# Kernel tuning notes

Measured on AMD Instinct MI355X. Metric: run time of the kernel, lower is better.

## Reference

```python
import jax, jax.numpy as jnp
import numpy as np

SIN, TEMB, EMB, S = 128, 512, 1024, 64
BATCH, T = 4, 4096


def setup_inputs() -> dict:
    key = jax.random.key(0)
    ks = jax.random.split(key, 16)

    def w(k, *shape):
        return jax.random.normal(k, shape, jnp.float32) / np.float32(np.sqrt(shape[0]))

    return {
        "time_embed": jax.random.normal(ks[0], (SIN,), jnp.float32),
        "x": jax.random.normal(ks[1], (BATCH, T, EMB), jnp.float32),
        "W1": w(ks[2], SIN, TEMB), "b1": jnp.zeros((TEMB,), jnp.float32),
        "W2": w(ks[3], TEMB, TEMB), "b2": jnp.zeros((TEMB,), jnp.float32),
        "WA": w(ks[4], TEMB, S), "bA": jnp.zeros((S,), jnp.float32),
        "WB": w(ks[5], TEMB, S, EMB), "bB": jnp.zeros((S, EMB), jnp.float32),
        "WC": w(ks[6], TEMB, EMB, S), "bC": jnp.zeros((EMB, S), jnp.float32),
        "WD": w(ks[7], TEMB, EMB), "bD": jnp.zeros((EMB,), jnp.float32),
        "Wdl": w(ks[8], TEMB, S), "bdl": jnp.zeros((S,), jnp.float32),
        "MA": w(ks[9], SIN, S), "mA": jnp.zeros((S,), jnp.float32),
        "MB": w(ks[10], SIN, S, EMB), "mB": jnp.zeros((S, EMB), jnp.float32),
        "MC": w(ks[11], SIN, EMB, S), "mC": jnp.zeros((EMB, S), jnp.float32),
        "MD": w(ks[12], SIN, EMB), "mD": jnp.zeros((EMB,), jnp.float32),
        "Mdl": w(ks[13], SIN, S), "mdl": jnp.zeros((S,), jnp.float32),
    }


def _ssm_forward(time_embed, x, W1, b1, W2, b2, WA, bA, WB, bB, WC, bC, WD, bD,
                 Wdl, bdl, MA, mA, MB, mB, MC, mC, MD, mD, Mdl, mdl):
    # time-dependent parameter generation
    t = jax.nn.silu(time_embed @ W1 + b1)
    t = t @ W2 + b2  # [TEMB]

    A_base = -jax.nn.softplus(t @ WA + bA)                       # [S]
    B_base = jnp.einsum('t,tse->se', t, WB) + bB                 # [S,E]
    C_base = jnp.einsum('t,tes->es', t, WC) + bC                 # [E,S]
    D_base = t @ WD + bD                                         # [E]
    delta_base = jax.nn.softplus(t @ Wdl + bdl) + 1e-4           # [S]

    A = A_base * jax.nn.sigmoid(time_embed @ MA + mA)
    Bm = B_base * jax.nn.sigmoid(jnp.einsum('t,tse->se', time_embed, MB) + mB)
    C = C_base * jax.nn.sigmoid(jnp.einsum('t,tes->es', time_embed, MC) + mC)
    D = D_base * jax.nn.sigmoid(time_embed @ MD + mD)
    delta = delta_base * jax.nn.sigmoid(time_embed @ Mdl + mdl)  # [S]

    A_bar = jnp.exp(delta * A)          # [S]
    B_bar = delta[:, None] * Bm         # [S,E]

    xt = jnp.swapaxes(x, 0, 1)          # [T,B,E]

    def step(h, x_t):                   # h: [B,S], x_t: [B,E]
        h_new = A_bar * h + x_t @ B_bar.T
        y = h_new @ C.T                 # [B,E]
        return h_new, y

    h0 = jnp.zeros((x.shape[0], A_bar.shape[0]), x.dtype)
    _, ys = jax.lax.scan(step, h0, xt)  # ys: [T,B,E]
    return jnp.swapaxes(ys, 0, 1) + D * x


def reference(time_embed, x, W1, b1, W2, b2, WA, bA, WB, bB, WC, bC, WD, bD,
              Wdl, bdl, MA, mA, MB, mB, MC, mC, MD, mD, Mdl, mdl):
    return _ssm_forward(time_embed, x, W1, b1, W2, b2, WA, bA, WB, bB, WC, bC,
                        WD, bD, Wdl, bdl, MA, mA, MB, mB, MC, mC, MD, mD, Mdl, mdl)
```

## Files before the change

### kernel.cpp

```cpp
#include <hip/hip_runtime.h>
#include <math.h>

#define SIN_ 128
#define TEMB_ 512
#define EMB_ 1024
#define S_ 64
#define B_ 4
#define T_ 4096
#define NROW (B_*T_)
#define L_ 32
#define NC_ (T_/L_)

#define GK 32
#define NSL 16
#define NCH 16
#define NGCH 4

#define WS_T1     0
#define WS_T2     512
#define WS_DELTA  1024
#define WS_ABAR   1088
#define WS_EL     1152
#define WS_FAC    1216
#define WS_D      3264
#define WS_BMTH   4288
#define WS_CTH    37056
#define WS_PD     69824
#define WS_PDG    86208
#define WS_PA     90304
#define WS_PDL    90432
#define WS_PBF    90560
#define WS_HLOCH  90560
#define WS_CHEND  1401280
#define WS_CARRY  1434048

__device__ __forceinline__ float sigmoidf_(float x){ return 1.f/(1.f+expf(-x)); }
__device__ __forceinline__ float softplusf_(float x){ return x>20.f ? x : log1pf(expf(x)); }
__device__ __forceinline__ float4 sig4_(float4 g){
  float4 r; r.x=sigmoidf_(g.x); r.y=sigmoidf_(g.y); r.z=sigmoidf_(g.z); r.w=sigmoidf_(g.w); return r;
}
__device__ __forceinline__ unsigned short f2bf(float x){
  unsigned int u = __float_as_uint(x);
  unsigned int r = (u + 0x7FFFu + ((u>>16)&1u)) >> 16;
  return (unsigned short)r;
}
__device__ __forceinline__ ushort4 pack4(float4 v){
  return make_ushort4(f2bf(v.x),f2bf(v.y),f2bf(v.z),f2bf(v.w));
}
__device__ __forceinline__ float bf2f(unsigned short h){
  return __uint_as_float(((unsigned int)h)<<16);
}

__global__ void k_t1(const float* __restrict__ te, const float* __restrict__ W1,
                     const float* __restrict__ b1, float* __restrict__ ws){
  __shared__ float ste[SIN_];
  int tid = threadIdx.x;
  ste[tid] = te[tid]; ste[tid+64] = te[tid+64];
  __syncthreads();
  int j = blockIdx.x*64 + tid;
  float a = b1[j];
  #pragma unroll 16
  for (int i=0;i<SIN_;i++) a += ste[i]*W1[i*TEMB_ + j];
  ws[WS_T1 + j] = a * sigmoidf_(a);
}

__global__ __launch_bounds__(512) void k_t2(const float* __restrict__ W2,
                                            const float* __restrict__ b2,
                                            float* __restrict__ ws){
  __shared__ float st1[TEMB_];
  __shared__ float red[8][64];
  int tid = threadIdx.x;
  st1[tid] = ws[WS_T1 + tid];
  __syncthreads();
  int jl = tid & 63, kc = tid >> 6;
  int j = blockIdx.x*64 + jl;
  float p = 0.f;
  #pragma unroll 8
  for (int i=0;i<64;i++){
    int k = kc*64 + i;
    p += st1[k]*W2[k*TEMB_ + j];
  }
  red[kc][jl] = p;
  __syncthreads();
  if (tid < 64){
    float a = b2[blockIdx.x*64 + tid];
    #pragma unroll
    for (int c=0;c<8;c++) a += red[c][tid];
    ws[WS_T2 + blockIdx.x*64 + tid] = a;
  }
}

__global__ __launch_bounds__(256,2) void k_partial(
    const float* __restrict__ te,
    const float* __restrict__ WB, const float* __restrict__ MB,
    const float* __restrict__ WC, const float* __restrict__ MC,
    const float* __restrict__ WD, const float* __restrict__ MD,
    const float* __restrict__ WA, const float* __restrict__ MA,
    const float* __restrict__ Wdl, const float* __restrict__ Mdl,
    float* __restrict__ ws){
  __shared__ float st2[TEMB_];
  __shared__ float ste[SIN_];
  int tid = threadIdx.x;
  st2[tid] = ws[WS_T2 + tid];
  st2[tid+256] = ws[WS_T2 + tid + 256];
  if (tid < SIN_) ste[tid] = te[tid];
  __syncthreads();
  unsigned short* pbf = (unsigned short*)(ws + WS_PBF);
  int bb = blockIdx.x;
  if (bb < 512){
    int r = bb>>8, rem = bb&255, j = rem>>4, c = rem&15;
    const float4* W4 = (const float4*)(r ? WC : WB);
    const float4* base = W4 + (size_t)(c*GK)*16384 + j*1024 + tid;
    const float* coef = st2 + c*GK;
    float4 a0={0,0,0,0}, a1={0,0,0,0}, a2={0,0,0,0}, a3={0,0,0,0};
    #pragma unroll 4
    for (int k=0;k<GK;k++){
      const float4* p = base + (size_t)k*16384;
      float4 w0=p[0], w1=p[256], w2=p[512], w3=p[768];
      float cv = coef[k];
      a0.x=fmaf(cv,w0.x,a0.x); a0.y=fmaf(cv,w0.y,a0.y); a0.z=fmaf(cv,w0.z,a0.z); a0.w=fmaf(cv,w0.w,a0.w);
      a1.x=fmaf(cv,w1.x,a1.x); a1.y=fmaf(cv,w1.y,a1.y); a1.z=fmaf(cv,w1.z,a1.z); a1.w=fmaf(cv,w1.w,a1.w);
      a2.x=fmaf(cv,w2.x,a2.x); a2.y=fmaf(cv,w2.y,a2.y); a2.z=fmaf(cv,w2.z,a2.z); a2.w=fmaf(cv,w2.w,a2.w);
      a3.x=fmaf(cv,w3.x,a3.x); a3.y=fmaf(cv,w3.y,a3.y); a3.z=fmaf(cv,w3.z,a3.z); a3.w=fmaf(cv,w3.w,a3.w);
    }
    ushort4* dst = (ushort4*)pbf + (size_t)((r*NSL+j)*NCH + c)*1024;
    dst[tid]     = pack4(a0);
    dst[tid+256] = pack4(a1);
    dst[tid+512] = pack4(a2);
    dst[tid+768] = pack4(a3);
  } else if (bb < 640){
    int g = bb-512, r = g>>6, rem = g&63, j = rem>>2, cg = rem&3;
    const float4* M4 = (const float4*)(r ? MC : MB);
    const float4* base = M4 + (size_t)(cg*GK)*16384 + j*1024 + tid;
    const float* coef = ste + cg*GK;
    float4 a0={0,0,0,0}, a1={0,0,0,0}, a2={0,0,0,0}, a3={0,0,0,0};
    #pragma unroll 4
    for (int k=0;k<GK;k++){
      const float4* p = base + (size_t)k*16384;
      float4 w0=p[0], w1=p[256], w2=p[512], w3=p[768];
      float cv = coef[k];
      a0.x=fmaf(cv,w0.x,a0.x); a0.y=fmaf(cv,w0.y,a0.y); a0.z=fmaf(cv,w0.z,a0.z); a0.w=fmaf(cv,w0.w,a0.w);
      a1.x=fmaf(cv,w1.x,a1.x); a1.y=fmaf(cv,w1.y,a1.y); a1.z=fmaf(cv,w1.z,a1.z); a1.w=fmaf(cv,w1.w,a1.w);
      a2.x=fmaf(cv,w2.x,a2.x); a2.y=fmaf(cv,w2.y,a2.y); a2.z=fmaf(cv,w2.z,a2.z); a2.w=fmaf(cv,w2.w,a2.w);
      a3.x=fmaf(cv,w3.x,a3.x); a3.y=fmaf(cv,w3.y,a3.y); a3.z=fmaf(cv,w3.z,a3.z); a3.w=fmaf(cv,w3.w,a3.w);
    }
    ushort4* dst = (ushort4*)pbf + (size_t)524288 + (size_t)((r*NSL+j)*NGCH + cg)*1024;
    dst[tid]     = pack4(a0);
    dst[tid+256] = pack4(a1);
    dst[tid+512] = pack4(a2);
    dst[tid+768] = pack4(a3);
  } else if (bb < 656){
    int c = bb-640;
    const float4* base = (const float4*)WD + (size_t)(c*GK)*256 + tid;
    const float* coef = st2 + c*GK;
    float4 a={0,0,0,0};
    #pragma unroll 4
    for (int k=0;k<GK;k++){
      float4 w = base[(size_t)k*256];
      float cv = coef[k];
      a.x=fmaf(cv,w.x,a.x); a.y=fmaf(cv,w.y,a.y); a.z=fmaf(cv,w.z,a.z); a.w=fmaf(cv,w.w,a.w);
    }
    ((float4*)(ws + WS_PD))[c*256 + tid] = a;
  } else if (bb < 660){
    int cg = bb-656;
    const float4* base = (const float4*)MD + (size_t)(cg*GK)*256 + tid;
    const float* coef = ste + cg*GK;
    float4 a={0,0,0,0};
    #pragma unroll 4
    for (int k=0;k<GK;k++){
      float4 w = base[(size_t)k*256];
      float cv = coef[k];
      a.x=fmaf(cv,w.x,a.x); a.y=fmaf(cv,w.y,a.y); a.z=fmaf(cv,w.z,a.z); a.w=fmaf(cv,w.w,a.w);
    }
    ((float4*)(ws + WS_PDG))[cg*256 + tid] = a;
  } else {
    const float* Wm = (bb==660) ? WA : Wdl;
    const float* Mm = (bb==660) ? MA : Mdl;
    int outbase = (bb==660) ? WS_PA : WS_PDL;
    __shared__ float red[16][68];
    int q = tid&15, kr = tid>>4;
    float4 acc={0,0,0,0};
    const float4* W4 = (const float4*)Wm;
    #pragma unroll 4
    for (int it=0; it<32; ++it){
      int k = it*16 + kr;
      float4 w = W4[k*16 + q];
      float cv = st2[k];
      acc.x=fmaf(cv,w.x,acc.x); acc.y=fmaf(cv,w.y,acc.y); acc.z=fmaf(cv,w.z,acc.z); acc.w=fmaf(cv,w.w,acc.w);
    }
    red[kr][4*q+0]=acc.x; red[kr][4*q+1]=acc.y; red[kr][4*q+2]=acc.z; red[kr][4*q+3]=acc.w;
    __syncthreads();
    if (tid < 64){
      float s = 0.f;
      #pragma unroll
      for (int g=0;g<16;g++) s += red[g][tid];
      ws[outbase + tid] = s;
    }
    __syncthreads();
    float4 gac={0,0,0,0};
    const float4* M4 = (const float4*)Mm;
    #pragma unroll 4
    for (int it=0; it<8; ++it){
      int k = it*16 + kr;
      float4 w = M4[k*16 + q];
      float cv = ste[k];
      gac.x=fmaf(cv,w.x,gac.x); gac.y=fmaf(cv,w.y,gac.y); gac.z=fmaf(cv,w.z,gac.z); gac.w=fmaf(cv,w.w,gac.w);
    }
    red[kr][4*q+0]=gac.x; red[kr][4*q+1]=gac.y; red[kr][4*q+2]=gac.z; red[kr][4*q+3]=gac.w;
    __syncthreads();
    if (tid < 64){
      float s = 0.f;
      #pragma unroll
      for (int g=0;g<16;g++) s += red[g][tid];
      ws[outbase + 64 + tid] = s;
    }
  }
}

__global__ __launch_bounds__(256) void k_finalize(
    const float* __restrict__ bB, const float* __restrict__ mB,
    const float* __restrict__ bC, const float* __restrict__ mC,
    const float* __restrict__ bD, const float* __restrict__ mD,
    const float* __restrict__ bA_, const float* __restrict__ mA_,
    const float* __restrict__ bdl, const float* __restrict__ mdl,
    float* __restrict__ ws){
  int tid = threadIdx.x, bb = blockIdx.x;
  const ushort4* pbf4 = (const ushort4*)(ws + WS_PBF);
  unsigned short* bmth = (unsigned short*)(ws + WS_BMTH);
  unsigned short* cth  = (unsigned short*)(ws + WS_CTH);
  if (bb < 128){
    int r = bb>>6;
    int q = (bb&63)*256 + tid;
    int j = q>>10, p = q&1023;
    float4 a = {0,0,0,0};
    size_t wbase = ((size_t)(r*NSL+j)*NCH)*1024 + p;
    #pragma unroll
    for (int c=0;c<NCH;c++){
      ushort4 v = pbf4[wbase + (size_t)c*1024];
      a.x += bf2f(v.x); a.y += bf2f(v.y); a.z += bf2f(v.z); a.w += bf2f(v.w);
    }
    float4 g = {0,0,0,0};
    size_t gbase = (size_t)524288 + ((size_t)(r*NSL+j)*NGCH)*1024 + p;
    #pragma unroll
    for (int cg=0;cg<NGCH;cg++){
      ushort4 v = pbf4[gbase + (size_t)cg*1024];
      g.x += bf2f(v.x); g.y += bf2f(v.y); g.z += bf2f(v.z); g.w += bf2f(v.w);
    }
    if (r == 0){
      float4 b4 = ((const float4*)bB)[q];
      float4 m4 = ((const float4*)mB)[q];
      float4 sg = sig4_(make_float4(g.x+m4.x, g.y+m4.y, g.z+m4.z, g.w+m4.w));
      float4 v = make_float4((a.x+b4.x)*sg.x,(a.y+b4.y)*sg.y,(a.z+b4.z)*sg.z,(a.w+b4.w)*sg.w);
      int o = q*4; int s = o>>10; int e = o&1023;
      bmth[(e+0)*64 + s] = f2bf(v.x);
      bmth[(e+1)*64 + s] = f2bf(v.y);
      bmth[(e+2)*64 + s] = f2bf(v.z);
      bmth[(e+3)*64 + s] = f2bf(v.w);
    } else {
      float4 b4 = ((const float4*)bC)[q];
      float4 m4 = ((const float4*)mC)[q];
      float4 sg = sig4_(make_float4(g.x+m4.x, g.y+m4.y, g.z+m4.z, g.w+m4.w));
      float4 v = make_float4((a.x+b4.x)*sg.x,(a.y+b4.y)*sg.y,(a.z+b4.z)*sg.z,(a.w+b4.w)*sg.w);
      int o = q*4; int e = o>>6; int s = o&63;
      cth[(s+0)*1024 + e] = f2bf(v.x);
      cth[(s+1)*1024 + e] = f2bf(v.y);
      cth[(s+2)*1024 + e] = f2bf(v.z);
      cth[(s+3)*1024 + e] = f2bf(v.w);
    }
  } else if (bb == 128){
    float4 a = {0,0,0,0};
    #pragma unroll
    for (int c=0;c<NCH;c++){
      float4 v = ((const float4*)(ws + WS_PD))[c*256 + tid];
      a.x+=v.x; a.y+=v.y; a.z+=v.z; a.w+=v.w;
    }
    float4 g = {0,0,0,0};
    #pragma unroll
    for (int cg=0;cg<NGCH;cg++){
      float4 v = ((const float4*)(ws + WS_PDG))[cg*256 + tid];
      g.x+=v.x; g.y+=v.y; g.z+=v.z; g.w+=v.w;
    }
    float4 b4 = ((const float4*)bD)[tid];
    float4 m4 = ((const float4*)mD)[tid];
    float4 sg = sig4_(make_float4(g.x+m4.x, g.y+m4.y, g.z+m4.z, g.w+m4.w));
    float4 v = make_float4((a.x+b4.x)*sg.x,(a.y+b4.y)*sg.y,(a.z+b4.z)*sg.z,(a.w+b4.w)*sg.w);
    ((float4*)(ws + WS_D))[tid] = v;
  } else {
    __shared__ float sda[64];
    if (tid < 64){
      int s = tid;
      float A = -softplusf_(ws[WS_PA+s] + bA_[s]) * sigmoidf_(ws[WS_PA+64+s] + mA_[s]);
      float delta = (softplusf_(ws[WS_PDL+s] + bdl[s]) + 1e-4f) * sigmoidf_(ws[WS_PDL+64+s] + mdl[s]);
      float da = delta * A;
      sda[s] = da;
      ws[WS_DELTA+s] = delta;
      ws[WS_ABAR+s]  = expf(da);
      ws[WS_EL+s]    = expf((float)L_*da);
    }
    __syncthreads();
    for (int idx=tid; idx<L_*S_; idx+=256){
      int tl = idx>>6, s = idx&63;
      ws[WS_FAC+idx] = expf((float)(tl+1)*sda[s]);
    }
  }
}

__global__ __launch_bounds__(256) void k_scan(const float* __restrict__ x, float* __restrict__ ws){
  __shared__ float Xs[32][68];
  __shared__ float BsT[64][68];
  __shared__ float Us[32][65];
  __shared__ float sdl[S_], sab[S_];
  int tid = threadIdx.x;
  int bb = blockIdx.x;
  int row0 = (bb>>7)*T_ + (bb&127)*L_;
  if (tid<64){ sdl[tid]=ws[WS_DELTA+tid]; sab[tid]=ws[WS_ABAR+tid]; }
  float acc[2][4];
  #pragma unroll
  for (int i=0;i<2;i++)
    #pragma unroll
    for (int j=0;j<4;j++) acc[i][j]=0.f;
  int ty = tid>>4, tx = tid&15;
  const float4* x4 = (const float4*)x;
  const ushort4* bm4 = (const ushort4*)(ws + WS_BMTH);
  for (int kk=0; kk<EMB_; kk+=64){
    #pragma unroll
    for (int t=0;t<2;t++){
      int fl = t*256+tid; int rr = fl>>4, cq = fl&15;
      float4 xv = x4[(size_t)(row0+rr)*256 + (kk>>2) + cq];
      *(float4*)&Xs[rr][cq*4] = xv;
    }
    #pragma unroll
    for (int t=0;t<4;t++){
      int fl = t*256+tid; int rr = fl>>4, cq = fl&15;
      ushort4 hv = bm4[(size_t)(kk+rr)*16 + cq];
      *(float4*)&BsT[rr][cq*4] = make_float4(bf2f(hv.x),bf2f(hv.y),bf2f(hv.z),bf2f(hv.w));
    }
    __syncthreads();
    #pragma unroll 8
    for (int k=0;k<64;k++){
      float4 b4 = *(const float4*)&BsT[k][4*tx];
      float x0 = Xs[2*ty+0][k], x1 = Xs[2*ty+1][k];
      acc[0][0]+=x0*b4.x; acc[0][1]+=x0*b4.y; acc[0][2]+=x0*b4.z; acc[0][3]+=x0*b4.w;
      acc[1][0]+=x1*b4.x; acc[1][1]+=x1*b4.y; acc[1][2]+=x1*b4.z; acc[1][3]+=x1*b4.w;
    }
    __syncthreads();
  }
  #pragma unroll
  for (int i=0;i<2;i++)
    #pragma unroll
    for (int j=0;j<4;j++)
      Us[2*ty+i][4*tx+j] = acc[i][j]*sdl[4*tx+j];
  __syncthreads();
  if (tid<64){
    unsigned short* hh = (unsigned short*)(ws + WS_HLOCH);
    int s = tid; float h = 0.f, ab = sab[s];
    #pragma unroll 8
    for (int t=0;t<L_;t++){
      h = fmaf(ab, h, Us[t][s]);
      hh[(size_t)(row0+t)*S_ + s] = f2bf(h);
    }
    ws[WS_CHEND + bb*S_ + s] = h;
  }
}

__global__ __launch_bounds__(256) void k_carry(float* __restrict__ ws){
  __shared__ float ch[B_*NC_*S_];
  int tid = threadIdx.x;
  const float4* src = (const float4*)(ws + WS_CHEND);
  float4* chv = (float4*)ch;
  for (int i=tid;i<8192;i+=256) chv[i] = src[i];
  __syncthreads();
  int b = tid>>6, s = tid&63;
  float el = ws[WS_EL + s];
  float carry = 0.f;
  #pragma unroll 8
  for (int c=0;c<NC_;c++){
    int idx = (b*NC_ + c)*S_ + s;
    float v = ch[idx];
    ch[idx] = carry;
    carry = fmaf(el, carry, v);
  }
  __syncthreads();
  float4* dst = (float4*)(ws + WS_CARRY);
  for (int i=tid;i<8192;i+=256) dst[i] = chv[i];
}

__global__ __launch_bounds__(256) void k_out(const float* __restrict__ x,
                                             const float* __restrict__ ws,
                                             float* __restrict__ out){
  __shared__ float Cts[64][68];
  __shared__ float Hs[64][68];
  int tid = threadIdx.x;
  int bb = blockIdx.x;
  int rt = bb & 255, et = bb >> 8;
  int row0 = rt*64, e0 = et*64;
  int b = row0 >> 12;
  int cbase = b*NC_ + ((row0 & (T_-1)) >> 5);
  const ushort4* hl4h = (const ushort4*)(ws + WS_HLOCH);
  const ushort4* cth4 = (const ushort4*)(ws + WS_CTH);
  const float4* fc4 = (const float4*)(ws + WS_FAC);
  const float4* cr4 = (const float4*)(ws + WS_CARRY);
  #pragma unroll
  for (int t=0;t<4;t++){
    int fl = t*256+tid; int rr = fl>>4, q = fl&15;
    ushort4 h4 = hl4h[(size_t)(row0+rr)*16 + q];
    float4 f = fc4[(rr & (L_-1))*16 + q];
    float4 c = cr4[(cbase + (rr>>5))*16 + q];
    float4 hv = make_float4(bf2f(h4.x)+f.x*c.x, bf2f(h4.y)+f.y*c.y,
                            bf2f(h4.z)+f.z*c.z, bf2f(h4.w)+f.w*c.w);
    *(float4*)&Hs[rr][q*4] = hv;
    ushort4 ct4 = cth4[(size_t)rr*256 + (e0>>2) + q];
    *(float4*)&Cts[rr][q*4] = make_float4(bf2f(ct4.x),bf2f(ct4.y),bf2f(ct4.z),bf2f(ct4.w));
  }
  __syncthreads();
  int ty = tid>>4, tx = tid&15;
  float acc[4][4];
  #pragma unroll
  for (int i=0;i<4;i++)
    #pragma unroll
    for (int j=0;j<4;j++) acc[i][j]=0.f;
  #pragma unroll 8
  for (int s=0;s<64;s++){
    float4 c4 = *(const float4*)&Cts[s][4*tx];
    float h0 = Hs[4*ty+0][s], h1 = Hs[4*ty+1][s], h2 = Hs[4*ty+2][s], h3 = Hs[4*ty+3][s];
    acc[0][0]+=h0*c4.x; acc[0][1]+=h0*c4.y; acc[0][2]+=h0*c4.z; acc[0][3]+=h0*c4.w;
    acc[1][0]+=h1*c4.x; acc[1][1]+=h1*c4.y; acc[1][2]+=h1*c4.z; acc[1][3]+=h1*c4.w;
    acc[2][0]+=h2*c4.x; acc[2][1]+=h2*c4.y; acc[2][2]+=h2*c4.z; acc[2][3]+=h2*c4.w;
    acc[3][0]+=h3*c4.x; acc[3][1]+=h3*c4.y; acc[3][2]+=h3*c4.z; acc[3][3]+=h3*c4.w;
  }
  float4 d4 = ((const float4*)(ws + WS_D))[(e0>>2) + tx];
  #pragma unroll
  for (int i=0;i<4;i++){
    int row = row0 + 4*ty + i;
    float4 x4v = reinterpret_cast<const float4*>(x + (size_t)row*EMB_ + e0)[tx];
    float4 o;
    o.x = acc[i][0] + d4.x*x4v.x;
    o.y = acc[i][1] + d4.y*x4v.y;
    o.z = acc[i][2] + d4.z*x4v.z;
    o.w = acc[i][3] + d4.w*x4v.w;
    reinterpret_cast<float4*>(out + (size_t)row*EMB_ + e0)[tx] = o;
  }
}

extern "C" void kernel_launch(void* const* d_in, const int* in_sizes, int n_in,
                              void* d_out, int out_size, void* d_ws, size_t ws_size,
                              hipStream_t stream){
  const float* te  = (const float*)d_in[0];
  const float* x   = (const float*)d_in[1];
  const float* W1  = (const float*)d_in[2];
  const float* b1  = (const float*)d_in[3];
  const float* W2  = (const float*)d_in[4];
  const float* b2  = (const float*)d_in[5];
  const float* WA  = (const float*)d_in[6];
  const float* bA  = (const float*)d_in[7];
  const float* WB  = (const float*)d_in[8];
  const float* bB  = (const float*)d_in[9];
  const float* WC  = (const float*)d_in[10];
  const float* bC  = (const float*)d_in[11];
  const float* WD  = (const float*)d_in[12];
  const float* bD  = (const float*)d_in[13];
  const float* Wdl = (const float*)d_in[14];
  const float* bdl = (const float*)d_in[15];
  const float* MA  = (const float*)d_in[16];
  const float* mA  = (const float*)d_in[17];
  const float* MB  = (const float*)d_in[18];
  const float* mB  = (const float*)d_in[19];
  const float* MC  = (const float*)d_in[20];
  const float* mC  = (const float*)d_in[21];
  const float* MD  = (const float*)d_in[22];
  const float* mD  = (const float*)d_in[23];
  const float* Mdl = (const float*)d_in[24];
  const float* mdl = (const float*)d_in[25];
  float* ws  = (float*)d_ws;
  float* out = (float*)d_out;

  k_t1<<<8,64,0,stream>>>(te, W1, b1, ws);
  k_t2<<<8,512,0,stream>>>(W2, b2, ws);
  k_partial<<<662,256,0,stream>>>(te, WB,MB, WC,MC, WD,MD, WA,MA, Wdl,Mdl, ws);
  k_finalize<<<130,256,0,stream>>>(bB,mB, bC,mC, bD,mD, bA,mA, bdl,mdl, ws);
  k_scan<<<512,256,0,stream>>>(x, ws);
  k_carry<<<1,256,0,stream>>>(ws);
  k_out<<<4096,256,0,stream>>>(x, ws, out);
}
```

Baseline: 187.0 us.

## Double scan chunk length, enlarge output tiles, and use nontemporal weight loads

Doubles the scan chunk length to 64 and enlarges the per-block tiles in the scan and output kernels, halving their block counts and the number of chunk carries to propagate. This is meant to improve register-level reuse of B and C and shrink the serial carry kernel, at the cost of fewer blocks for occupancy and more registers per thread. The large weight reductions in the parameter kernel now use nontemporal vector loads and vector FMA syntax, aiming to avoid polluting the cache with streamed weights. Workspace offsets are shifted to fit the larger factor table.

```diff
diff --git a/kernel.cpp b/kernel.cpp
--- a/kernel.cpp
+++ b/kernel.cpp
@@ -8,7 +8,7 @@
 #define B_ 4
 #define T_ 4096
 #define NROW (B_*T_)
-#define L_ 32
+#define L_ 64
 #define NC_ (T_/L_)
 
 #define GK 32
@@ -22,17 +22,19 @@
 #define WS_ABAR   1088
 #define WS_EL     1152
 #define WS_FAC    1216
-#define WS_D      3264
-#define WS_BMTH   4288
-#define WS_CTH    37056
-#define WS_PD     69824
-#define WS_PDG    86208
-#define WS_PA     90304
-#define WS_PDL    90432
-#define WS_PBF    90560
-#define WS_HLOCH  90560
-#define WS_CHEND  1401280
-#define WS_CARRY  1434048
+#define WS_D      5312
+#define WS_BMTH   6336
+#define WS_CTH    39104
+#define WS_PD     71872
+#define WS_PDG    88256
+#define WS_PA     92352
+#define WS_PDL    92480
+#define WS_PBF    92608
+#define WS_HLOCH  92608
+#define WS_CHEND  1403328
+#define WS_CARRY  1419712
+
+typedef float nt4 __attribute__((ext_vector_type(4)));
 
 __device__ __forceinline__ float sigmoidf_(float x){ return 1.f/(1.f+expf(-x)); }
 __device__ __forceinline__ float softplusf_(float x){ return x>20.f ? x : log1pf(expf(x)); }
@@ -44,11 +46,14 @@
   unsigned int r = (u + 0x7FFFu + ((u>>16)&1u)) >> 16;
   return (unsigned short)r;
 }
-__device__ __forceinline__ ushort4 pack4(float4 v){
+__device__ __forceinline__ ushort4 pack4nt(nt4 v){
   return make_ushort4(f2bf(v.x),f2bf(v.y),f2bf(v.z),f2bf(v.w));
 }
 __device__ __forceinline__ float bf2f(unsigned short h){
   return __uint_as_float(((unsigned int)h)<<16);
+}
+__device__ __forceinline__ nt4 ntload(const float4* p){
+  return __builtin_nontemporal_load((const nt4*)p);
 }
 
 __global__ void k_t1(const float* __restrict__ te, const float* __restrict__ W1,
@@ -112,67 +117,61 @@
     const float4* W4 = (const float4*)(r ? WC : WB);
     const float4* base = W4 + (size_t)(c*GK)*16384 + j*1024 + tid;
     const float* coef = st2 + c*GK;
-    float4 a0={0,0,0,0}, a1={0,0,0,0}, a2={0,0,0,0}, a3={0,0,0,0};
+    nt4 a0={0,0,0,0}, a1={0,0,0,0}, a2={0,0,0,0}, a3={0,0,0,0};
     #pragma unroll 4
     for (int k=0;k<GK;k++){
       const float4* p = base + (size_t)k*16384;
-      float4 w0=p[0], w1=p[256], w2=p[512], w3=p[768];
+      nt4 w0=ntload(p), w1=ntload(p+256), w2=ntload(p+512), w3=ntload(p+768);
       float cv = coef[k];
-      a0.x=fmaf(cv,w0.x,a0.x); a0.y=fmaf(cv,w0.y,a0.y); a0.z=fmaf(cv,w0.z,a0.z); a0.w=fmaf(cv,w0.w,a0.w);
-      a1.x=fmaf(cv,w1.x,a1.x); a1.y=fmaf(cv,w1.y,a1.y); a1.z=fmaf(cv,w1.z,a1.z); a1.w=fmaf(cv,w1.w,a1.w);
-      a2.x=fmaf(cv,w2.x,a2.x); a2.y=fmaf(cv,w2.y,a2.y); a2.z=fmaf(cv,w2.z,a2.z); a2.w=fmaf(cv,w2.w,a2.w);
-      a3.x=fmaf(cv,w3.x,a3.x); a3.y=fmaf(cv,w3.y,a3.y); a3.z=fmaf(cv,w3.z,a3.z); a3.w=fmaf(cv,w3.w,a3.w);
+      a0 += cv*w0; a1 += cv*w1; a2 += cv*w2; a3 += cv*w3;
     }
     ushort4* dst = (ushort4*)pbf + (size_t)((r*NSL+j)*NCH + c)*1024;
-    dst[tid]     = pack4(a0);
-    dst[tid+256] = pack4(a1);
-    dst[tid+512] = pack4(a2);
-    dst[tid+768] = pack4(a3);
+    dst[tid]     = pack4nt(a0);
+    dst[tid+256] = pack4nt(a1);
+    dst[tid+512] = pack4nt(a2);
+    dst[tid+768] = pack4nt(a3);
   } else if (bb < 640){
     int g = bb-512, r = g>>6, rem = g&63, j = rem>>2, cg = rem&3;
     const float4* M4 = (const float4*)(r ? MC : MB);
     const float4* base = M4 + (size_t)(cg*GK)*16384 + j*1024 + tid;
     const float* coef = ste + cg*GK;
-    float4 a0={0,0,0,0}, a1={0,0,0,0}, a2={0,0,0,0}, a3={0,0,0,0};
+    nt4 a0={0,0,0,0}, a1={0,0,0,0}, a2={0,0,0,0}, a3={0,0,0,0};
     #pragma unroll 4
     for (int k=0;k<GK;k++){
       const float4* p = base + (size_t)k*16384;
-      float4 w0=p[0], w1=p[256], w2=p[512], w3=p[768];
+      nt4 w0=ntload(p), w1=ntload(p+256), w2=ntload(p+512), w3=ntload(p+768);
       float cv = coef[k];
-      a0.x=fmaf(cv,w0.x,a0.x); a0.y=fmaf(cv,w0.y,a0.y); a0.z=fmaf(cv,w0.z,a0.z); a0.w=fmaf(cv,w0.w,a0.w);
-      a1.x=fmaf(cv,w1.x,a1.x); a1.y=fmaf(cv,w1.y,a1.y); a1.z=fmaf(cv,w1.z,a1.z); a1.w=fmaf(cv,w1.w,a1.w);
-      a2.x=fmaf(cv,w2.x,a2.x); a2.y=fmaf(cv,w2.y,a2.y); a2.z=fmaf(cv,w2.z,a2.z); a2.w=fmaf(cv,w2.w,a2.w);
-      a3.x=fmaf(cv,w3.x,a3.x); a3.y=fmaf(cv,w3.y,a3.y); a3.z=fmaf(cv,w3.z,a3.z); a3.w=fmaf(cv,w3.w,a3.w);
+      a0 += cv*w0; a1 += cv*w1; a2 += cv*w2; a3 += cv*w3;
     }
     ushort4* dst = (ushort4*)pbf + (size_t)524288 + (size_t)((r*NSL+j)*NGCH + cg)*1024;
-    dst[tid]     = pack4(a0);
-    dst[tid+256] = pack4(a1);
-    dst[tid+512] = pack4(a2);
-    dst[tid+768] = pack4(a3);
+    dst[tid]     = pack4nt(a0);
+    dst[tid+256] = pack4nt(a1);
+    dst[tid+512] = pack4nt(a2);
+    dst[tid+768] = pack4nt(a3);
   } else if (bb < 656){
     int c = bb-640;
     const float4* base = (const float4*)WD + (size_t)(c*GK)*256 + tid;
     const float* coef = st2 + c*GK;
-    float4 a={0,0,0,0};
+    nt4 a={0,0,0,0};
     #pragma unroll 4
     for (int k=0;k<GK;k++){
-      float4 w = base[(size_t)k*256];
-      float cv = coef[k];
-      a.x=fmaf(cv,w.x,a.x); a.y=fmaf(cv,w.y,a.y); a.z=fmaf(cv,w.z,a.z); a.w=fmaf(cv,w.w,a.w);
-    }
-    ((float4*)(ws + WS_PD))[c*256 + tid] = a;
+      nt4 w = ntload(base + (size_t)k*256);
+      a += coef[k]*w;
+    }
+    float4 af = make_float4(a.x,a.y,a.z,a.w);
+    ((float4*)(ws + WS_PD))[c*256 + tid] = af;
   } else if (bb < 660){
     int cg = bb-656;
     const float4* base = (const float4*)MD + (size_t)(cg*GK)*256 + tid;
     const float* coef = ste + cg*GK;
-    float4 a={0,0,0,0};
+    nt4 a={0,0,0,0};
     #pragma unroll 4
     for (int k=0;k<GK;k++){
-      float4 w = base[(size_t)k*256];
-      float cv = coef[k];
-      a.x=fmaf(cv,w.x,a.x); a.y=fmaf(cv,w.y,a.y); a.z=fmaf(cv,w.z,a.z); a.w=fmaf(cv,w.w,a.w);
-    }
-    ((float4*)(ws + WS_PDG))[cg*256 + tid] = a;
+      nt4 w = ntload(base + (size_t)k*256);
+      a += coef[k]*w;
+    }
+    float4 af = make_float4(a.x,a.y,a.z,a.w);
+    ((float4*)(ws + WS_PDG))[cg*256 + tid] = af;
   } else {
     const float* Wm = (bb==660) ? WA : Wdl;
     const float* Mm = (bb==660) ? MA : Mdl;
@@ -306,17 +305,17 @@
 }
 
 __global__ __launch_bounds__(256) void k_scan(const float* __restrict__ x, float* __restrict__ ws){
-  __shared__ float Xs[32][68];
+  __shared__ float Xs[64][68];
   __shared__ float BsT[64][68];
-  __shared__ float Us[32][65];
+  __shared__ float Us[64][65];
   __shared__ float sdl[S_], sab[S_];
   int tid = threadIdx.x;
   int bb = blockIdx.x;
-  int row0 = (bb>>7)*T_ + (bb&127)*L_;
+  int row0 = (bb>>6)*T_ + (bb&63)*L_;
   if (tid<64){ sdl[tid]=ws[WS_DELTA+tid]; sab[tid]=ws[WS_ABAR+tid]; }
-  float acc[2][4];
-  #pragma unroll
-  for (int i=0;i<2;i++)
+  float acc[4][4];
+  #pragma unroll
+  for (int i=0;i<4;i++)
     #pragma unroll
     for (int j=0;j<4;j++) acc[i][j]=0.f;
   int ty = tid>>4, tx = tid&15;
@@ -324,14 +323,10 @@
   const ushort4* bm4 = (const ushort4*)(ws + WS_BMTH);
   for (int kk=0; kk<EMB_; kk+=64){
     #pragma unroll
-    for (int t=0;t<2;t++){
+    for (int t=0;t<4;t++){
       int fl = t*256+tid; int rr = fl>>4, cq = fl&15;
       float4 xv = x4[(size_t)(row0+rr)*256 + (kk>>2) + cq];
       *(float4*)&Xs[rr][cq*4] = xv;
-    }
-    #pragma unroll
-    for (int t=0;t<4;t++){
-      int fl = t*256+tid; int rr = fl>>4, cq = fl&15;
       ushort4 hv = bm4[(size_t)(kk+rr)*16 + cq];
       *(float4*)&BsT[rr][cq*4] = make_float4(bf2f(hv.x),bf2f(hv.y),bf2f(hv.z),bf2f(hv.w));
     }
@@ -339,17 +334,19 @@
     #pragma unroll 8
     for (int k=0;k<64;k++){
       float4 b4 = *(const float4*)&BsT[k][4*tx];
-      float x0 = Xs[2*ty+0][k], x1 = Xs[2*ty+1][k];
+      float x0 = Xs[4*ty+0][k], x1 = Xs[4*ty+1][k], x2 = Xs[4*ty+2][k], x3 = Xs[4*ty+3][k];
       acc[0][0]+=x0*b4.x; acc[0][1]+=x0*b4.y; acc[0][2]+=x0*b4.z; acc[0][3]+=x0*b4.w;
       acc[1][0]+=x1*b4.x; acc[1][1]+=x1*b4.y; acc[1][2]+=x1*b4.z; acc[1][3]+=x1*b4.w;
-    }
-    __syncthreads();
-  }
-  #pragma unroll
-  for (int i=0;i<2;i++)
+      acc[2][0]+=x2*b4.x; acc[2][1]+=x2*b4.y; acc[2][2]+=x2*b4.z; acc[2][3]+=x2*b4.w;
+      acc[3][0]+=x3*b4.x; acc[3][1]+=x3*b4.y; acc[3][2]+=x3*b4.z; acc[3][3]+=x3*b4.w;
+    }
+    __syncthreads();
+  }
+  #pragma unroll
+  for (int i=0;i<4;i++)
     #pragma unroll
     for (int j=0;j<4;j++)
-      Us[2*ty+i][4*tx+j] = acc[i][j]*sdl[4*tx+j];
+      Us[4*ty+i][4*tx+j] = acc[i][j]*sdl[4*tx+j];
   __syncthreads();
   if (tid<64){
     unsigned short* hh = (unsigned short*)(ws + WS_HLOCH);
@@ -368,7 +365,7 @@
   int tid = threadIdx.x;
   const float4* src = (const float4*)(ws + WS_CHEND);
   float4* chv = (float4*)ch;
-  for (int i=tid;i<8192;i+=256) chv[i] = src[i];
+  for (int i=tid;i<4096;i+=256) chv[i] = src[i];
   __syncthreads();
   int b = tid>>6, s = tid&63;
   float el = ws[WS_EL + s];
@@ -382,56 +379,60 @@
   }
   __syncthreads();
   float4* dst = (float4*)(ws + WS_CARRY);
-  for (int i=tid;i<8192;i+=256) dst[i] = chv[i];
+  for (int i=tid;i<4096;i+=256) dst[i] = chv[i];
 }
 
 __global__ __launch_bounds__(256) void k_out(const float* __restrict__ x,
                                              const float* __restrict__ ws,
                                              float* __restrict__ out){
   __shared__ float Cts[64][68];
-  __shared__ float Hs[64][68];
+  __shared__ float Hs[128][68];
   int tid = threadIdx.x;
   int bb = blockIdx.x;
-  int rt = bb & 255, et = bb >> 8;
-  int row0 = rt*64, e0 = et*64;
+  int rt = bb & 127, et = bb >> 7;
+  int row0 = rt*128, e0 = et*64;
   int b = row0 >> 12;
-  int cbase = b*NC_ + ((row0 & (T_-1)) >> 5);
+  int cbase = b*NC_ + ((row0 & (T_-1)) >> 6);
   const ushort4* hl4h = (const ushort4*)(ws + WS_HLOCH);
   const ushort4* cth4 = (const ushort4*)(ws + WS_CTH);
   const float4* fc4 = (const float4*)(ws + WS_FAC);
   const float4* cr4 = (const float4*)(ws + WS_CARRY);
   #pragma unroll
-  for (int t=0;t<4;t++){
+  for (int t=0;t<8;t++){
     int fl = t*256+tid; int rr = fl>>4, q = fl&15;
     ushort4 h4 = hl4h[(size_t)(row0+rr)*16 + q];
     float4 f = fc4[(rr & (L_-1))*16 + q];
-    float4 c = cr4[(cbase + (rr>>5))*16 + q];
+    float4 c = cr4[(cbase + (rr>>6))*16 + q];
     float4 hv = make_float4(bf2f(h4.x)+f.x*c.x, bf2f(h4.y)+f.y*c.y,
                             bf2f(h4.z)+f.z*c.z, bf2f(h4.w)+f.w*c.w);
     *(float4*)&Hs[rr][q*4] = hv;
+  }
+  #pragma unroll
+  for (int t=0;t<4;t++){
+    int fl = t*256+tid; int rr = fl>>4, q = fl&15;
     ushort4 ct4 = cth4[(size_t)rr*256 + (e0>>2) + q];
     *(float4*)&Cts[rr][q*4] = make_float4(bf2f(ct4.x),bf2f(ct4.y),bf2f(ct4.z),bf2f(ct4.w));
   }
   __syncthreads();
   int ty = tid>>4, tx = tid&15;
-  float acc[4][4];
-  #pragma unroll
-  for (int i=0;i<4;i++)
+  float acc[8][4];
+  #pragma unroll
+  for (int i=0;i<8;i++)
     #pragma unroll
     for (int j=0;j<4;j++) acc[i][j]=0.f;
-  #pragma unroll 8
+  #pragma unroll 4
   for (int s=0;s<64;s++){
     float4 c4 = *(const float4*)&Cts[s][4*tx];
-    float h0 = Hs[4*ty+0][s], h1 = Hs[4*ty+1][s], h2 = Hs[4*ty+2][s], h3 = Hs[4*ty+3][s];
-    acc[0][0]+=h0*c4.x; acc[0][1]+=h0*c4.y; acc[0][2]+=h0*c4.z; acc[0][3]+=h0*c4.w;
-    acc[1][0]+=h1*c4.x; acc[1][1]+=h1*c4.y; acc[1][2]+=h1*c4.z; acc[1][3]+=h1*c4.w;
-    acc[2][0]+=h2*c4.x; acc[2][1]+=h2*c4.y; acc[2][2]+=h2*c4.z; acc[2][3]+=h2*c4.w;
-    acc[3][0]+=h3*c4.x; acc[3][1]+=h3*c4.y; acc[3][2]+=h3*c4.z; acc[3][3]+=h3*c4.w;
+    #pragma unroll
+    for (int i=0;i<8;i++){
+      float hv = Hs[8*ty+i][s];
+      acc[i][0]+=hv*c4.x; acc[i][1]+=hv*c4.y; acc[i][2]+=hv*c4.z; acc[i][3]+=hv*c4.w;
+    }
   }
   float4 d4 = ((const float4*)(ws + WS_D))[(e0>>2) + tx];
   #pragma unroll
-  for (int i=0;i<4;i++){
-    int row = row0 + 4*ty + i;
+  for (int i=0;i<8;i++){
+    int row = row0 + 8*ty + i;
     float4 x4v = reinterpret_cast<const float4*>(x + (size_t)row*EMB_ + e0)[tx];
     float4 o;
     o.x = acc[i][0] + d4.x*x4v.x;
@@ -478,7 +479,7 @@
   k_t2<<<8,512,0,stream>>>(W2, b2, ws);
   k_partial<<<662,256,0,stream>>>(te, WB,MB, WC,MC, WD,MD, WA,MA, Wdl,Mdl, ws);
   k_finalize<<<130,256,0,stream>>>(bB,mB, bC,mC, bD,mD, bA,mA, bdl,mdl, ws);
-  k_scan<<<512,256,0,stream>>>(x, ws);
+  k_scan<<<256,256,0,stream>>>(x, ws);
   k_carry<<<1,256,0,stream>>>(ws);
-  k_out<<<4096,256,0,stream>>>(x, ws, out);
-}
+  k_out<<<2048,256,0,stream>>>(x, ws, out);
+}
```

Result: faster. 159.6 us (-14.6%).
